# Optimization experiments

Measured on AMD Instinct MI355X. Metric: run time of the kernel, lower is better.

## Reference

```python
import jax, jax.numpy as jnp
import numpy as np

HEADS = 8
DIM_HEAD = 64


def setup_inputs() -> dict:
    key = jax.random.key(0)
    ks = jax.random.split(key, 10)
    B, NQ, NK, D, INNER = 4, 2048, 2048, 1024, HEADS * DIM_HEAD
    w_scale = 0.02
    return {
        "x": jax.random.normal(ks[0], (B, NQ, D), jnp.float32),
        "context": jax.random.normal(ks[1], (B, NK, D), jnp.float32),
        "wq": jax.random.normal(ks[2], (D, INNER), jnp.float32) * w_scale,
        "bq": jax.random.normal(ks[3], (INNER,), jnp.float32) * w_scale,
        "wk": jax.random.normal(ks[4], (D, INNER), jnp.float32) * w_scale,
        "bk": jax.random.normal(ks[5], (INNER,), jnp.float32) * w_scale,
        "wv": jax.random.normal(ks[6], (D, INNER), jnp.float32) * w_scale,
        "bv": jax.random.normal(ks[7], (INNER,), jnp.float32) * w_scale,
        "wo": jax.random.normal(ks[8], (INNER, D), jnp.float32) * w_scale,
        "bo": jax.random.normal(ks[9], (D,), jnp.float32) * w_scale,
    }


def _split_heads(t):
    # [b, n, h*d] -> [b, h, n, d]
    b, n, _ = t.shape
    return t.reshape(b, n, HEADS, DIM_HEAD).transpose(0, 2, 1, 3)


def reference(x, context, wq, bq, wk, bk, wv, bv, wo, bo):
    scale = DIM_HEAD ** -0.5
    q = _split_heads(x @ wq + bq)        # [b, h, nq, d]
    k = _split_heads(context @ wk + bk)  # [b, h, nk, d]
    v = _split_heads(context @ wv + bv)  # [b, h, nk, d]
    sim = jnp.einsum('bhid,bhjd->bhij', q, k) * scale  # full score matrix, as in original
    attn = jax.nn.softmax(sim, axis=-1)
    out = jnp.einsum('bhij,bhjd->bhid', attn, v)       # [b, h, nq, d]
    b, h, n, d = out.shape
    out = out.transpose(0, 2, 1, 3).reshape(b, n, h * d)
    return out @ wo + bo
```

## Files before the change

### kernel.cpp

```cpp
#include <hip/hip_runtime.h>
#include <hip/hip_bf16.h>

typedef __attribute__((ext_vector_type(8))) short short8;
typedef __attribute__((ext_vector_type(4))) float f32x4;
typedef __attribute__((ext_vector_type(2))) unsigned uint2u;

__device__ __forceinline__ short f2bf(float f) {
  union { float f; unsigned u; } x; x.f = f;
  unsigned r = x.u + 0x7fffu + ((x.u >> 16) & 1u);
  return (short)(r >> 16);
}

__device__ __forceinline__ unsigned cvt_pk_bf16(float a, float b) {
  unsigned r;
  asm("v_cvt_pk_bf16_f32 %0, %1, %2" : "=v"(r) : "v"(a), "v"(b));
  return r;
}

__device__ __forceinline__ void gload16(const short* g, short* l) {
  __builtin_amdgcn_global_load_lds(
      (const __attribute__((address_space(1))) unsigned*)g,
      (__attribute__((address_space(3))) unsigned*)l, 16, 0, 0);
}

__device__ __forceinline__ void barrier_lgkm() {
  asm volatile("s_waitcnt lgkmcnt(0)" ::: "memory");
  __builtin_amdgcn_s_barrier();
}

__global__ void cast2_bf16_kernel(const float* __restrict__ a,
                                  const float* __restrict__ b,
                                  short* __restrict__ dst) {
  int i = (blockIdx.x * 256 + threadIdx.x) * 4;
  const float* s = (i < (1 << 23)) ? a : b;
  int j = i & ((1 << 23) - 1);
  float4 f = *(const float4*)(s + j);
  union { short s[4]; uint2 u; } o;
  o.s[0] = f2bf(f.x); o.s[1] = f2bf(f.y);
  o.s[2] = f2bf(f.z); o.s[3] = f2bf(f.w);
  *(uint2*)(dst + i) = o.u;
}

__global__ __launch_bounds__(256) void transpose_cast4_kernel(
    const float* __restrict__ wq, const float* __restrict__ wk,
    const float* __restrict__ wv, const float* __restrict__ wo,
    short* __restrict__ wqt, short* __restrict__ wkt,
    short* __restrict__ wvt, short* __restrict__ wot) {
  __shared__ short tile[64][72];
  int z = blockIdx.z;
  const float* src = (z == 0) ? wq : (z == 1) ? wk : (z == 2) ? wv : wo;
  short* dst = (z == 0) ? wqt : (z == 1) ? wkt : (z == 2) ? wvt : wot;
  int R = (z < 3) ? 1024 : 512, C = (z < 3) ? 512 : 1024;
  int tpc = C >> 6;
  int bx = blockIdx.x % tpc, by = blockIdx.x / tpc;
  int r0 = by * 64, c0 = bx * 64;
  int tx = threadIdx.x & 15, ty = threadIdx.x >> 4;
#pragma unroll
  for (int i = 0; i < 4; i++) {
    int r = i * 16 + ty;
    float4 f = *(const float4*)(src + (size_t)(r0 + r) * C + c0 + tx * 4);
    union { short s[4]; uint2 u; } o;
    o.s[0] = f2bf(f.x); o.s[1] = f2bf(f.y);
    o.s[2] = f2bf(f.z); o.s[3] = f2bf(f.w);
    *(uint2*)&tile[r][tx * 4] = o.u;
  }
  __syncthreads();
#pragma unroll
  for (int i = 0; i < 4; i++) {
    int c = i * 16 + ty;
    union { short s[4]; uint2 u; } o;
#pragma unroll
    for (int k = 0; k < 4; k++) o.s[k] = tile[tx * 4 + k][c];
    *(uint2*)(dst + (size_t)(c0 + c) * R + r0 + tx * 4) = o.u;
  }
}

__device__ __forceinline__ void gemm_core(
    const short* __restrict__ A, const short* __restrict__ Bt, int K,
    int mblk, int nblk, short* sA, short* sB, f32x4 (&acc)[4][4]) {
  int tid = threadIdx.x;
  int lane = tid & 63, wave = tid >> 6;
  int quad = lane >> 4, l15 = lane & 15;
  int wm = (wave >> 1) * 64, wn = (wave & 1) * 64;
  int sub = lane >> 3, e8 = lane & 7;
  int swz = (e8 ^ sub) << 3;
  int s0 = (quad ^ (l15 & 7)) << 3;
  const short* Ag = A + (size_t)(mblk + 32 * wave + sub) * K + swz;
  const short* Bg = Bt + (size_t)(nblk + 32 * wave + sub) * K + swz;
  short* Al = sA + 4 * wave * 512;
  short* Bl = sB + 4 * wave * 512;

  for (int k0 = 0; k0 < K; k0 += 64) {
    __syncthreads();
#pragma unroll
    for (int t = 0; t < 4; t++) {
      gload16(Ag + (size_t)(8 * t) * K + k0, Al + t * 512);
      gload16(Bg + (size_t)(8 * t) * K + k0, Bl + t * 512);
    }
    __syncthreads();
#pragma unroll
    for (int h = 0; h < 2; h++) {
      int so = s0 ^ (h << 5);
      short8 af[4], bf[4];
#pragma unroll
      for (int mt = 0; mt < 4; mt++)
        af[mt] = *(const short8*)(&sA[(wm + mt * 16 + l15) * 64 + so]);
#pragma unroll
      for (int nt = 0; nt < 4; nt++)
        bf[nt] = *(const short8*)(&sB[(wn + nt * 16 + l15) * 64 + so]);
#pragma unroll
      for (int mt = 0; mt < 4; mt++)
#pragma unroll
        for (int nt = 0; nt < 4; nt++)
          acc[mt][nt] = __builtin_amdgcn_mfma_f32_16x16x32_bf16(
              af[mt], bf[nt], acc[mt][nt], 0, 0, 0);
    }
  }
}

__global__ __launch_bounds__(256) void gemm_qkv(
    const short* __restrict__ xb, const short* __restrict__ cb,
    const short* __restrict__ wqt, const short* __restrict__ wkt,
    const short* __restrict__ wvt,
    const float* __restrict__ bq, const float* __restrict__ bk,
    const float* __restrict__ bv,
    short* __restrict__ Qb, short* __restrict__ Kb, short* __restrict__ Vt) {
  __shared__ __align__(16) short sA[128 * 64];
  __shared__ __align__(16) short sB[128 * 64];
  int z = blockIdx.z;
  const short* A  = (z == 0) ? xb : cb;
  const short* Bt = (z == 0) ? wqt : (z == 1) ? wkt : wvt;
  const float* bias = (z == 0) ? bq : (z == 1) ? bk : bv;
  short* out = (z == 0) ? Qb : (z == 1) ? Kb : Vt;
  float scale = (z == 0) ? 0.18033688011112042f : 1.0f;
  int mblk = blockIdx.x * 128, nblk = blockIdx.y * 128;
  f32x4 acc[4][4] = {};
  gemm_core(A, Bt, 1024, mblk, nblk, sA, sB, acc);

  int lane = threadIdx.x & 63, wave = threadIdx.x >> 6;
  int quad = lane >> 4, l15 = lane & 15;
  int wm = (wave >> 1) * 64, wn = (wave & 1) * 64;
#pragma unroll
  for (int nt = 0; nt < 4; nt++) {
    int col = nblk + wn + nt * 16 + l15;
    float bias_v = bias[col];
    int h = col >> 6, dh = col & 63;
#pragma unroll
    for (int mt = 0; mt < 4; mt++)
#pragma unroll
      for (int r = 0; r < 4; r++) {
        int row = mblk + wm + mt * 16 + quad * 4 + r;
        float v = (acc[mt][nt][r] + bias_v) * scale;
        int b = row >> 11, n = row & 2047;
        size_t base = ((size_t)(b * 8 + h)) << 17;
        size_t idx = (z == 2) ? base + ((size_t)dh << 11) + n
                              : base + ((size_t)n << 6) + dh;
        out[idx] = f2bf(v);
      }
  }
}

__global__ __launch_bounds__(256) void gemm_out(
    const short* __restrict__ Ob, const short* __restrict__ wot,
    const float* __restrict__ bo, float* __restrict__ out) {
  __shared__ __align__(16) short sA[128 * 64];
  __shared__ __align__(16) short sB[128 * 64];
  int mblk = blockIdx.x * 128, nblk = blockIdx.y * 128;
  f32x4 acc[4][4] = {};
  gemm_core(Ob, wot, 512, mblk, nblk, sA, sB, acc);
  int lane = threadIdx.x & 63, wave = threadIdx.x >> 6;
  int quad = lane >> 4, l15 = lane & 15;
  int wm = (wave >> 1) * 64, wn = (wave & 1) * 64;
#pragma unroll
  for (int nt = 0; nt < 4; nt++) {
    int col = nblk + wn + nt * 16 + l15;
    float bias_v = bo[col];
#pragma unroll
    for (int mt = 0; mt < 4; mt++)
#pragma unroll
      for (int r = 0; r < 4; r++) {
        int row = mblk + wm + mt * 16 + quad * 4 + r;
        out[(size_t)row * 1024 + col] = acc[mt][nt][r] + bias_v;
      }
  }
}

__global__ __launch_bounds__(256, 4) void attn_kernel(
    const short* __restrict__ Qb, const short* __restrict__ Kb,
    const short* __restrict__ Vt, float* __restrict__ Op,
    float* __restrict__ Ls) {
  __shared__ __align__(16) short sK[2 * 64 * 64];
  __shared__ __align__(16) short sV[2 * 64 * 64];
  int tid = threadIdx.x;
  int lane = tid & 63, wave = tid >> 6;
  int quad = lane >> 4, l15 = lane & 15;
  int bh = blockIdx.x & 31;
  int qt = (blockIdx.x >> 5) & 15;
  int ks = blockIdx.x >> 9;
  const short* Qp = Qb + ((size_t)bh << 17);
  const short* Kp = Kb + ((size_t)bh << 17);
  const short* Vp = Vt + ((size_t)bh << 17);
  int qrow0 = qt * 128 + wave * 32;
  int t0 = ks * 16;

  short8 qf[2][2];
#pragma unroll
  for (int g = 0; g < 2; g++) {
    const short* qrow = Qp + (size_t)(qrow0 + g * 16 + l15) * 64;
    qf[g][0] = *(const short8*)(qrow + quad * 8);
    qf[g][1] = *(const short8*)(qrow + 32 + quad * 8);
  }

  int jk0 = 2 * wave, jk1 = 2 * wave + 1;
  int sub = lane >> 3;
  int e8  = lane & 7;
  int swz = (e8 ^ sub) << 3;
  const short* kg0 = Kp + (size_t)(8 * jk0 + sub) * 64 + e8 * 8;
  const short* kg1 = Kp + (size_t)(8 * jk1 + sub) * 64 + e8 * 8;
  const short* vg0 = Vp + (size_t)(8 * jk0 + sub) * 2048 + e8 * 8;
  const short* vg1 = Vp + (size_t)(8 * jk1 + sub) * 2048 + e8 * 8;
  int kw0 = (8 * jk0 + sub) * 64 + swz;
  int kw1 = (8 * jk1 + sub) * 64 + swz;

  int s0 = (quad ^ (l15 & 7)) << 3;
  int s1 = s0 ^ 32;

  f32x4 o[2][4] = {};
  float lsum[2] = {0.f, 0.f};

  uint4 rk0 = *(const uint4*)(kg0 + (size_t)t0 * 4096);
  uint4 rk1 = *(const uint4*)(kg1 + (size_t)t0 * 4096);
  uint4 rv0 = *(const uint4*)(vg0 + (size_t)t0 * 64);
  uint4 rv1 = *(const uint4*)(vg1 + (size_t)t0 * 64);
  *(uint4*)(sK + kw0) = rk0; *(uint4*)(sK + kw1) = rk1;
  *(uint4*)(sV + kw0) = rv0; *(uint4*)(sV + kw1) = rv1;
  rk0 = *(const uint4*)(kg0 + (size_t)(t0 + 1) * 4096);
  rk1 = *(const uint4*)(kg1 + (size_t)(t0 + 1) * 4096);
  rv0 = *(const uint4*)(vg0 + (size_t)(t0 + 1) * 64);
  rv1 = *(const uint4*)(vg1 + (size_t)(t0 + 1) * 64);
  barrier_lgkm();

  for (int it = 0; it < 16; ++it) {
    const short* sKr = sK + (it & 1) * 4096;
    const short* sVr = sV + (it & 1) * 4096;
    if (it < 15) {
      short* sKw = sK + ((it & 1) ^ 1) * 4096;
      short* sVw = sV + ((it & 1) ^ 1) * 4096;
      *(uint4*)(sKw + kw0) = rk0; *(uint4*)(sKw + kw1) = rk1;
      *(uint4*)(sVw + kw0) = rv0; *(uint4*)(sVw + kw1) = rv1;
      if (it < 14) {
        size_t ko = (size_t)(t0 + it + 2) * 4096;
        size_t vo = (size_t)(t0 + it + 2) * 64;
        rk0 = *(const uint4*)(kg0 + ko); rk1 = *(const uint4*)(kg1 + ko);
        rv0 = *(const uint4*)(vg0 + vo); rv1 = *(const uint4*)(vg1 + vo);
      }
    }
    unsigned xp[2][4][2];
#pragma unroll
    for (int jt = 0; jt < 4; jt++) {
      short8 k0 = *(const short8*)(&sKr[(jt * 16 + l15) * 64 + s0]);
      short8 k1 = *(const short8*)(&sKr[(jt * 16 + l15) * 64 + s1]);
#pragma unroll
      for (int g = 0; g < 2; g++) {
        f32x4 zz = {0.f, 0.f, 0.f, 0.f};
        __builtin_amdgcn_s_setprio(1);
        zz = __builtin_amdgcn_mfma_f32_16x16x32_bf16(k0, qf[g][0], zz, 0, 0, 0);
        f32x4 st = __builtin_amdgcn_mfma_f32_16x16x32_bf16(k1, qf[g][1], zz, 0, 0, 0);
        __builtin_amdgcn_s_setprio(0);
        float p0 = exp2f(st[0]), p1 = exp2f(st[1]);
        float p2 = exp2f(st[2]), p3 = exp2f(st[3]);
        lsum[g] += (p0 + p1) + (p2 + p3);
        xp[g][jt][0] = cvt_pk_bf16(p0, p1);
        xp[g][jt][1] = cvt_pk_bf16(p2, p3);
      }
    }
    short8 pf[2][2];
#pragma unroll
    for (int g = 0; g < 2; g++) {
#pragma unroll
      for (int hb = 0; hb < 2; hb++) {
        unsigned x0 = xp[g][2 * hb][0], x1 = xp[g][2 * hb][1];
        unsigned x2 = xp[g][2 * hb + 1][0], x3 = xp[g][2 * hb + 1][1];
        uint2u r1 = __builtin_amdgcn_permlane32_swap(x0, x2, false, false);
        uint2u r2 = __builtin_amdgcn_permlane16_swap(r1[0], r1[1], false, false);
        uint2u r3 = __builtin_amdgcn_permlane32_swap(x1, x3, false, false);
        uint2u r4 = __builtin_amdgcn_permlane16_swap(r3[0], r3[1], false, false);
        union { unsigned u[4]; short8 s; } P;
        P.u[0] = r2[0]; P.u[1] = r4[0]; P.u[2] = r2[1]; P.u[3] = r4[1];
        pf[g][hb] = P.s;
      }
    }
    __builtin_amdgcn_s_setprio(1);
#pragma unroll
    for (int nt = 0; nt < 4; nt++) {
      short8 v0 = *(const short8*)(&sVr[(nt * 16 + l15) * 64 + s0]);
      short8 v1 = *(const short8*)(&sVr[(nt * 16 + l15) * 64 + s1]);
#pragma unroll
      for (int g = 0; g < 2; g++) {
        o[g][nt] = __builtin_amdgcn_mfma_f32_16x16x32_bf16(v0, pf[g][0], o[g][nt], 0, 0, 0);
        o[g][nt] = __builtin_amdgcn_mfma_f32_16x16x32_bf16(v1, pf[g][1], o[g][nt], 0, 0, 0);
      }
    }
    __builtin_amdgcn_s_setprio(0);
    if (it < 15) barrier_lgkm();
  }

  int b = bh >> 3, h = bh & 7;
  float* Opb = Op + ((size_t)ks << 22);
#pragma unroll
  for (int g = 0; g < 2; g++) {
    float l = lsum[g];
    l += __shfl_xor(l, 16, 64);
    l += __shfl_xor(l, 32, 64);
    if (lane < 16)
      Ls[(ks << 16) + (bh << 11) + qrow0 + g * 16 + lane] = l;
    size_t rowbase = ((size_t)b * 2048 + qrow0 + g * 16 + l15) * 512 + h * 64 + quad * 4;
#pragma unroll
    for (int nt = 0; nt < 4; nt++)
      *(f32x4*)(Opb + rowbase + nt * 16) = o[g][nt];
  }
}

__global__ __launch_bounds__(256) void combine_kernel(
    const float* __restrict__ Op, const float* __restrict__ Ls,
    short* __restrict__ Ob) {
  int i = (blockIdx.x * 256 + threadIdx.x) * 8;
  int row = i >> 9, colb = i & 511;
  int b = row >> 11, n = row & 2047, h = colb >> 6;
  int lsi = (((b << 3) + h) << 11) + n;
  float inv = 1.0f / (Ls[lsi] + Ls[65536 + lsi]);
  const float* p0 = Op + i;
  const float* p1 = Op + (1u << 22) + i;
  float4 a0 = *(const float4*)p0, a1 = *(const float4*)(p0 + 4);
  float4 b0 = *(const float4*)p1, b1 = *(const float4*)(p1 + 4);
  union { short s[8]; uint4 u; } o;
  o.s[0] = f2bf((a0.x + b0.x) * inv);
  o.s[1] = f2bf((a0.y + b0.y) * inv);
  o.s[2] = f2bf((a0.z + b0.z) * inv);
  o.s[3] = f2bf((a0.w + b0.w) * inv);
  o.s[4] = f2bf((a1.x + b1.x) * inv);
  o.s[5] = f2bf((a1.y + b1.y) * inv);
  o.s[6] = f2bf((a1.z + b1.z) * inv);
  o.s[7] = f2bf((a1.w + b1.w) * inv);
  *(uint4*)(Ob + i) = o.u;
}

extern "C" void kernel_launch(void* const* d_in, const int* in_sizes, int n_in,
                              void* d_out, int out_size, void* d_ws, size_t ws_size,
                              hipStream_t stream) {
  const float* x   = (const float*)d_in[0];
  const float* ctx = (const float*)d_in[1];
  const float* wq  = (const float*)d_in[2];
  const float* bq  = (const float*)d_in[3];
  const float* wk  = (const float*)d_in[4];
  const float* bk  = (const float*)d_in[5];
  const float* wv  = (const float*)d_in[6];
  const float* bv  = (const float*)d_in[7];
  const float* wo  = (const float*)d_in[8];
  const float* bo  = (const float*)d_in[9];
  float* out = (float*)d_out;
  char* ws = (char*)d_ws;

  short* xb  = (short*)(ws);
  short* cb  = (short*)(ws + (16ull << 20));
  short* wqt = (short*)(ws + (32ull << 20));
  short* wkt = (short*)(ws + (33ull << 20));
  short* wvt = (short*)(ws + (34ull << 20));
  short* wot = (short*)(ws + (35ull << 20));
  short* Qb  = (short*)(ws + (36ull << 20));
  short* Kb  = (short*)(ws + (44ull << 20));
  short* Vt  = (short*)(ws + (52ull << 20));
  short* Ob  = (short*)(ws + (60ull << 20));
  float* Op  = (float*)(ws);
  float* Ls  = (float*)(ws + (32ull << 20));

  cast2_bf16_kernel<<<16384, 256, 0, stream>>>(x, ctx, xb);
  transpose_cast4_kernel<<<dim3(128, 1, 4), 256, 0, stream>>>(
      wq, wk, wv, wo, wqt, wkt, wvt, wot);
  gemm_qkv<<<dim3(64, 4, 3), 256, 0, stream>>>(xb, cb, wqt, wkt, wvt,
                                               bq, bk, bv, Qb, Kb, Vt);
  attn_kernel<<<1024, 256, 0, stream>>>(Qb, Kb, Vt, Op, Ls);
  combine_kernel<<<2048, 256, 0, stream>>>(Op, Ls, Ob);
  gemm_out<<<dim3(64, 8), 256, 0, stream>>>(Ob, wot, bo, out);
}
```

Baseline: 251.3 us.

## Split attention key range four ways and combine four partial results

Doubles the split-K factor of the attention kernel from 2 to 4, so each block handles 8 key tiles and the grid grows to 2048 blocks for more parallelism. The extra partial outputs go to the final output buffer as scratch space, and the combine kernel sums four partials and four row sums. In exchange the combine step reads twice as much fp32 data, and each block runs a shorter loop that amortises its prologue and Q load over fewer tiles.

```diff
diff --git a/kernel.cpp b/kernel.cpp
--- a/kernel.cpp
+++ b/kernel.cpp
@@ -187,8 +187,8 @@
 
 __global__ __launch_bounds__(256, 4) void attn_kernel(
     const short* __restrict__ Qb, const short* __restrict__ Kb,
-    const short* __restrict__ Vt, float* __restrict__ Op,
-    float* __restrict__ Ls) {
+    const short* __restrict__ Vt, float* __restrict__ Op01,
+    float* __restrict__ Op23, float* __restrict__ Ls) {
   __shared__ __align__(16) short sK[2 * 64 * 64];
   __shared__ __align__(16) short sV[2 * 64 * 64];
   int tid = threadIdx.x;
@@ -201,7 +201,7 @@
   const short* Kp = Kb + ((size_t)bh << 17);
   const short* Vp = Vt + ((size_t)bh << 17);
   int qrow0 = qt * 128 + wave * 32;
-  int t0 = ks * 16;
+  int t0 = ks * 8;
 
   short8 qf[2][2];
 #pragma unroll
@@ -240,15 +240,15 @@
   rv1 = *(const uint4*)(vg1 + (size_t)(t0 + 1) * 64);
   barrier_lgkm();
 
-  for (int it = 0; it < 16; ++it) {
+  for (int it = 0; it < 8; ++it) {
     const short* sKr = sK + (it & 1) * 4096;
     const short* sVr = sV + (it & 1) * 4096;
-    if (it < 15) {
+    if (it < 7) {
       short* sKw = sK + ((it & 1) ^ 1) * 4096;
       short* sVw = sV + ((it & 1) ^ 1) * 4096;
       *(uint4*)(sKw + kw0) = rk0; *(uint4*)(sKw + kw1) = rk1;
       *(uint4*)(sVw + kw0) = rv0; *(uint4*)(sVw + kw1) = rv1;
-      if (it < 14) {
+      if (it < 6) {
         size_t ko = (size_t)(t0 + it + 2) * 4096;
         size_t vo = (size_t)(t0 + it + 2) * 64;
         rk0 = *(const uint4*)(kg0 + ko); rk1 = *(const uint4*)(kg1 + ko);
@@ -302,11 +302,12 @@
       }
     }
     __builtin_amdgcn_s_setprio(0);
-    if (it < 15) barrier_lgkm();
+    if (it < 7) barrier_lgkm();
   }
 
   int b = bh >> 3, h = bh & 7;
-  float* Opb = Op + ((size_t)ks << 22);
+  float* Opb = (ks < 2) ? (Op01 + ((size_t)ks << 22))
+                        : (Op23 + ((size_t)(ks - 2) << 22));
 #pragma unroll
   for (int g = 0; g < 2; g++) {
     float l = lsum[g];
@@ -322,26 +323,31 @@
 }
 
 __global__ __launch_bounds__(256) void combine_kernel(
-    const float* __restrict__ Op, const float* __restrict__ Ls,
-    short* __restrict__ Ob) {
+    const float* __restrict__ Op01, const float* __restrict__ Op23,
+    const float* __restrict__ Ls, short* __restrict__ Ob) {
   int i = (blockIdx.x * 256 + threadIdx.x) * 8;
   int row = i >> 9, colb = i & 511;
   int b = row >> 11, n = row & 2047, h = colb >> 6;
   int lsi = (((b << 3) + h) << 11) + n;
-  float inv = 1.0f / (Ls[lsi] + Ls[65536 + lsi]);
-  const float* p0 = Op + i;
-  const float* p1 = Op + (1u << 22) + i;
+  float inv = 1.0f / (Ls[lsi] + Ls[65536 + lsi] +
+                      Ls[131072 + lsi] + Ls[196608 + lsi]);
+  const float* p0 = Op01 + i;
+  const float* p1 = Op01 + (1u << 22) + i;
+  const float* p2 = Op23 + i;
+  const float* p3 = Op23 + (1u << 22) + i;
   float4 a0 = *(const float4*)p0, a1 = *(const float4*)(p0 + 4);
   float4 b0 = *(const float4*)p1, b1 = *(const float4*)(p1 + 4);
+  float4 c0 = *(const float4*)p2, c1 = *(const float4*)(p2 + 4);
+  float4 d0 = *(const float4*)p3, d1 = *(const float4*)(p3 + 4);
   union { short s[8]; uint4 u; } o;
-  o.s[0] = f2bf((a0.x + b0.x) * inv);
-  o.s[1] = f2bf((a0.y + b0.y) * inv);
-  o.s[2] = f2bf((a0.z + b0.z) * inv);
-  o.s[3] = f2bf((a0.w + b0.w) * inv);
-  o.s[4] = f2bf((a1.x + b1.x) * inv);
-  o.s[5] = f2bf((a1.y + b1.y) * inv);
-  o.s[6] = f2bf((a1.z + b1.z) * inv);
-  o.s[7] = f2bf((a1.w + b1.w) * inv);
+  o.s[0] = f2bf((a0.x + b0.x + c0.x + d0.x) * inv);
+  o.s[1] = f2bf((a0.y + b0.y + c0.y + d0.y) * inv);
+  o.s[2] = f2bf((a0.z + b0.z + c0.z + d0.z) * inv);
+  o.s[3] = f2bf((a0.w + b0.w + c0.w + d0.w) * inv);
+  o.s[4] = f2bf((a1.x + b1.x + c1.x + d1.x) * inv);
+  o.s[5] = f2bf((a1.y + b1.y + c1.y + d1.y) * inv);
+  o.s[6] = f2bf((a1.z + b1.z + c1.z + d1.z) * inv);
+  o.s[7] = f2bf((a1.w + b1.w + c1.w + d1.w) * inv);
   *(uint4*)(Ob + i) = o.u;
 }
 
@@ -371,15 +377,16 @@
   short* Kb  = (short*)(ws + (44ull << 20));
   short* Vt  = (short*)(ws + (52ull << 20));
   short* Ob  = (short*)(ws + (60ull << 20));
-  float* Op  = (float*)(ws);
-  float* Ls  = (float*)(ws + (32ull << 20));
+  float* Op01 = (float*)(ws);
+  float* Op23 = out;
+  float* Ls   = (float*)(ws + (32ull << 20));
 
   cast2_bf16_kernel<<<16384, 256, 0, stream>>>(x, ctx, xb);
   transpose_cast4_kernel<<<dim3(128, 1, 4), 256, 0, stream>>>(
       wq, wk, wv, wo, wqt, wkt, wvt, wot);
   gemm_qkv<<<dim3(64, 4, 3), 256, 0, stream>>>(xb, cb, wqt, wkt, wvt,
                                                bq, bk, bv, Qb, Kb, Vt);
-  attn_kernel<<<1024, 256, 0, stream>>>(Qb, Kb, Vt, Op, Ls);
-  combine_kernel<<<2048, 256, 0, stream>>>(Op, Ls, Ob);
+  attn_kernel<<<2048, 256, 0, stream>>>(Qb, Kb, Vt, Op01, Op23, Ls);
+  combine_kernel<<<2048, 256, 0, stream>>>(Op01, Op23, Ls, Ob);
   gemm_out<<<dim3(64, 8), 256, 0, stream>>>(Ob, wot, bo, out);
 }
```

After: 262.7 us. +4.5%, slower.
